# Kernel optimization log

Hardware: AMD Instinct MI355X
Metric: run time of the kernel (lower is better)

## Reference

```python
import jax, jax.numpy as jnp
import numpy as np

CLIP_TANH = 10.0
M_CHECKS, N_VARS = 256, 512   # parity-check matrix shape
ROW_W = 8                     # ones per check row -> E = 256*8 = 2048 edges
BATCH = 16384


def _build_masks():
    """Tanner-graph connectivity masks, as in init_w_skipconn2even / initialize_w_v2c."""
    rng = np.random.default_rng(0)
    pcm = np.zeros((M_CHECKS, N_VARS), np.float32)
    for r in range(M_CHECKS):
        pcm[r, rng.choice(N_VARS, ROW_W, replace=False)] = 1.0
    checks, variables = np.nonzero(pcm)  # edge list, row-major order, length E
    E = checks.size
    # edge e' feeds edge e iff same variable node, different check node
    same_var = variables[:, None] == variables[None, :]
    diff_chk = checks[:, None] != checks[None, :]
    w_odd2even_mask = (same_var & diff_chk).astype(np.float32)               # [E, E]
    # variable v feeds every edge incident to it
    w_skip_mask = (np.arange(N_VARS)[:, None] == variables[None, :]).astype(np.float32)  # [N, E]
    return jnp.asarray(w_odd2even_mask), jnp.asarray(w_skip_mask), E


def setup_inputs() -> dict:
    key = jax.random.key(0)
    w_o2e_mask, w_skip_mask, E = _build_masks()
    k = jax.random.split(key, 5)
    return {
        "x": jax.random.normal(k[0], (BATCH, E), jnp.float32),          # edge messages
        "llr": jax.random.normal(k[1], (BATCH, N_VARS), jnp.float32),   # channel LLRs
        "u": jax.random.uniform(k[2], (E,), jnp.float32),               # dropout uniforms
        "odd_weights": 0.05 * jax.random.normal(k[3], (E, E), jnp.float32),
        "llr_weights": 1.0 + 0.05 * jax.random.normal(k[4], (N_VARS, E), jnp.float32),
        "dropout_logits": 10.0 * jnp.ones((E,), jnp.float32),           # 10000*LOGITS_INIT analogue (sigmoid ~ 1)
        "w_odd2even_mask": w_o2e_mask,
        "w_skipconn2even_mask": w_skip_mask,
    }


def reference(x, llr, u, odd_weights, llr_weights, dropout_logits,
              w_odd2even_mask, w_skipconn2even_mask):
    # TEST-phase forward, mask_only=False
    total_mask = w_odd2even_mask * odd_weights                        # [E, E], very sparse support
    z = (u < jax.nn.sigmoid(dropout_logits)).astype(x.dtype)          # Bernoulli gate per source edge
    mask_after_dropout = total_mask * z[:, None]                      # row-wise gating
    msg = x @ mask_after_dropout                                      # [B, E]
    skip = llr @ (w_skipconn2even_mask * llr_weights)                 # [B, E]
    odd_clamp = jnp.clip(msg + skip, -CLIP_TANH, CLIP_TANH)
    return jnp.tanh(0.5 * odd_clamp)
```

## Files before the change

### kernel.cpp

```cpp
#include <hip/hip_runtime.h>
#include <hip/hip_bf16.h>

constexpr int E     = 2048;
constexpr int NVARS = 512;
constexpr int DMAX  = 20;
constexpr int TB    = 8;
constexpr int NT    = 512;

__device__ __forceinline__ unsigned bf16hi(float f) {
    const unsigned uu = __float_as_uint(f);
    return (uu + 0x7FFFu + ((uu >> 16) & 1u)) & 0xFFFF0000u;
}
__device__ __forceinline__ unsigned cvtpk(float lo, float hi) {
    unsigned r;
    asm("v_cvt_pk_bf16_f32 %0, %1, %2" : "=v"(r) : "v"(lo), "v"(hi));
    return r;
}
__device__ __forceinline__ float bl(unsigned q) { return __uint_as_float(q << 16); }
__device__ __forceinline__ float bh(unsigned q) { return __uint_as_float(q & 0xFFFF0000u); }

__global__ __launch_bounds__(256)
void k_vsrc(const float* __restrict__ skip_mask,
            const float* __restrict__ llr_w,
            unsigned short* __restrict__ vsrc,
            float* __restrict__ skw)
{
    const int col = blockIdx.x * 256 + threadIdx.x;
    const int v0  = blockIdx.y * (NVARS / 32);
    for (int v = v0; v < v0 + NVARS / 32; ++v) {
        const float m = skip_mask[(size_t)v * E + col];
        if (m != 0.0f) {
            vsrc[col] = (unsigned short)v;
            skw [col] = m * llr_w[(size_t)v * E + col];
        }
    }
}

__global__ __launch_bounds__(64)
void k_pervar(const unsigned short* __restrict__ vsrc,
              const float* __restrict__ skw,
              const float* __restrict__ odd_w,
              const float* __restrict__ u,
              const float* __restrict__ logits,
              uint4*  __restrict__ wtc,
              float4* __restrict__ hdr,
              int*    __restrict__ nitems)
{
    __shared__ unsigned short vs[E];
    __shared__ int deg[NVARS];
    __shared__ unsigned short mem[DMAX];
    __shared__ float zf[DMAX];
    __shared__ float sks[DMAX];

    const int v   = blockIdx.x;
    const int tid = threadIdx.x;

    for (int i = tid; i < E / 8; i += 64)
        ((uint4*)vs)[i] = ((const uint4*)vsrc)[i];
    for (int i = tid; i < NVARS; i += 64) deg[i] = 0;
    __syncthreads();
    for (int i = tid; i < E; i += 64) atomicAdd(&deg[vs[i]], 1);
    __syncthreads();

    const int dv = deg[v];

    int itot = 0, ib = 0, wb = 0;
    for (int i = tid; i < NVARS; i += 64) {
        const int d2 = deg[i];
        if (!d2) continue;
        const int dc = (d2 < DMAX) ? d2 : DMAX;
        const int ic = (dc + 3) >> 2;
        itot += ic;
        if (dv > 0 && (d2 < dv || (d2 == dv && i < v))) { ib += ic; wb += dc * ic; }
    }
    #pragma unroll
    for (int o = 32; o; o >>= 1) {
        itot += __shfl_xor(itot, o);
        ib   += __shfl_xor(ib,   o);
        wb   += __shfl_xor(wb,   o);
    }
    if (v == 0 && tid == 0) nitems[0] = itot;
    if (!dv) return;
    const int de = (dv < DMAX) ? dv : DMAX;
    const int ic = (de + 3) >> 2;

    int cnt = 0;
    for (int c = 0; c < E / 64; ++c) {
        const int e = c * 64 + tid;
        const bool m = ((int)vs[e] == v);
        const unsigned long long bal = __ballot(m);
        if (m) {
            const int pos = cnt + __popcll(bal & ((1ull << tid) - 1ull));
            if (pos < DMAX) mem[pos] = (unsigned short)e;
        }
        cnt += __popcll(bal);
    }
    __syncthreads();

    if (tid < de) {
        const int m = mem[tid];
        const float sig = 1.0f / (1.0f + __expf(-logits[m]));
        zf [tid] = (u[m] < sig) ? 1.0f : 0.0f;
        sks[tid] = skw[m];
    }
    __syncthreads();

    if (tid < ic) {
        const int o0 = tid * 4;
        float s0 = 0, s1 = 0, s2 = 0, s3 = 0;
        unsigned c0 = 0xFFFFu, c1 = 0xFFFFu, c2 = 0xFFFFu, c3 = 0xFFFFu;
        if (o0 + 0 < de) { s0 = sks[o0 + 0]; c0 = mem[o0 + 0]; }
        if (o0 + 1 < de) { s1 = sks[o0 + 1]; c1 = mem[o0 + 1]; }
        if (o0 + 2 < de) { s2 = sks[o0 + 2]; c2 = mem[o0 + 2]; }
        if (o0 + 3 < de) { s3 = sks[o0 + 3]; c3 = mem[o0 + 3]; }
        hdr[2 * (ib + tid)]     = make_float4(s0, s1, s2, s3);
        hdr[2 * (ib + tid) + 1] = make_float4(
            __uint_as_float(c0 | (c1 << 16)),
            __uint_as_float(c2 | (c3 << 16)),
            __uint_as_float((unsigned)(wb + tid * de)),
            __uint_as_float((unsigned)v | ((unsigned)de << 16)));
    }

    for (int idx = tid; idx < de * ic; idx += 64) {
        const int k = idx / de;
        const int j = idx - k * de;
        const int src = mem[j];
        unsigned g[4];
        #pragma unroll
        for (int q = 0; q < 4; ++q) {
            const int o = 4 * k + q;
            float ww = 0.0f;
            if (o < de && o != j)
                ww = odd_w[(size_t)src * E + mem[o]] * zf[j];
            g[q] = bf16hi(ww) | (unsigned)src;
        }
        wtc[wb + idx] = make_uint4(g[0], g[1], g[2], g[3]);
    }
}

__device__ __forceinline__ float th(float s) {
    float c = fminf(fmaxf(s, -10.0f), 10.0f);
    float t = __expf(c);
    return (t - 1.0f) * __frcp_rn(t + 1.0f);
}

__global__ __launch_bounds__(NT, 6)
void fused_main(const float* __restrict__ x,
                const float* __restrict__ llr,
                const uint4*  __restrict__ wtc,
                const float4* __restrict__ hdr,
                const int*    __restrict__ nitems,
                float* __restrict__ out)
{
    __shared__ uint4 xs[E];
    __shared__ uint4 ls[NVARS];

    const int b0 = blockIdx.x * TB;
    const int t  = threadIdx.x;

    {
        const float4* xr = (const float4*)(x + (size_t)b0 * E);
        const float4 r0 = xr[0 * (E / 4) + t];
        const float4 r1 = xr[1 * (E / 4) + t];
        const float4 r2 = xr[2 * (E / 4) + t];
        const float4 r3 = xr[3 * (E / 4) + t];
        const float4 r4 = xr[4 * (E / 4) + t];
        const float4 r5 = xr[5 * (E / 4) + t];
        const float4 r6 = xr[6 * (E / 4) + t];
        const float4 r7 = xr[7 * (E / 4) + t];
        xs[4 * t + 0] = make_uint4(cvtpk(r0.x, r1.x), cvtpk(r2.x, r3.x),
                                   cvtpk(r4.x, r5.x), cvtpk(r6.x, r7.x));
        xs[4 * t + 1] = make_uint4(cvtpk(r0.y, r1.y), cvtpk(r2.y, r3.y),
                                   cvtpk(r4.y, r5.y), cvtpk(r6.y, r7.y));
        xs[4 * t + 2] = make_uint4(cvtpk(r0.z, r1.z), cvtpk(r2.z, r3.z),
                                   cvtpk(r4.z, r5.z), cvtpk(r6.z, r7.z));
        xs[4 * t + 3] = make_uint4(cvtpk(r0.w, r1.w), cvtpk(r2.w, r3.w),
                                   cvtpk(r4.w, r5.w), cvtpk(r6.w, r7.w));
    }
    {
        const float* lr = llr + (size_t)b0 * NVARS;
        ls[t] = make_uint4(cvtpk(lr[t],             lr[NVARS + t]),
                           cvtpk(lr[2 * NVARS + t], lr[3 * NVARS + t]),
                           cvtpk(lr[4 * NVARS + t], lr[5 * NVARS + t]),
                           cvtpk(lr[6 * NVARS + t], lr[7 * NVARS + t]));
    }
    __syncthreads();

    const int nit = nitems[0];

    unsigned sst[2][4][4];
    unsigned scc[2][2];

    #pragma unroll
    for (int r = 0; r < 2; ++r) {
        scc[r][0] = 0xFFFFFFFFu;
        scc[r][1] = 0xFFFFFFFFu;
        const int it = r * NT + t;
        if (it < nit) {
            const float4 ha = hdr[2 * it];
            const uint4  hb = ((const uint4*)hdr)[2 * it + 1];
            const unsigned woff = hb.z;
            const int v = hb.w & 0xFFFF;
            const int d = hb.w >> 16;

            const uint4 lvq = ls[v];
            const float lf0 = bl(lvq.x), lf1 = bh(lvq.x);
            const float lf2 = bl(lvq.y), lf3 = bh(lvq.y);
            const float lf4 = bl(lvq.z), lf5 = bh(lvq.z);
            const float lf6 = bl(lvq.w), lf7 = bh(lvq.w);

            float a[4][8];
            #pragma unroll
            for (int ii = 0; ii < 4; ++ii) {
                const float sk = (ii == 0) ? ha.x : (ii == 1) ? ha.y
                               : (ii == 2) ? ha.z : ha.w;
                a[ii][0] = sk * lf0; a[ii][1] = sk * lf1;
                a[ii][2] = sk * lf2; a[ii][3] = sk * lf3;
                a[ii][4] = sk * lf4; a[ii][5] = sk * lf5;
                a[ii][6] = sk * lf6; a[ii][7] = sk * lf7;
            }

            const uint4* wp = wtc + woff;
            for (int j = 0; j < d; ++j) {
                const uint4 g = wp[j];
                const int   s = (int)(g.x & 0x7FFu);
                const uint4 xv = xs[s];
                const float w0 = bh(g.x), w1 = bh(g.y);
                const float w2 = bh(g.z), w3 = bh(g.w);
                const float xf0 = bl(xv.x), xf1 = bh(xv.x);
                const float xf2 = bl(xv.y), xf3 = bh(xv.y);
                const float xf4 = bl(xv.z), xf5 = bh(xv.z);
                const float xf6 = bl(xv.w), xf7 = bh(xv.w);
                a[0][0] += w0 * xf0; a[0][1] += w0 * xf1;
                a[0][2] += w0 * xf2; a[0][3] += w0 * xf3;
                a[0][4] += w0 * xf4; a[0][5] += w0 * xf5;
                a[0][6] += w0 * xf6; a[0][7] += w0 * xf7;
                a[1][0] += w1 * xf0; a[1][1] += w1 * xf1;
                a[1][2] += w1 * xf2; a[1][3] += w1 * xf3;
                a[1][4] += w1 * xf4; a[1][5] += w1 * xf5;
                a[1][6] += w1 * xf6; a[1][7] += w1 * xf7;
                a[2][0] += w2 * xf0; a[2][1] += w2 * xf1;
                a[2][2] += w2 * xf2; a[2][3] += w2 * xf3;
                a[2][4] += w2 * xf4; a[2][5] += w2 * xf5;
                a[2][6] += w2 * xf6; a[2][7] += w2 * xf7;
                a[3][0] += w3 * xf0; a[3][1] += w3 * xf1;
                a[3][2] += w3 * xf2; a[3][3] += w3 * xf3;
                a[3][4] += w3 * xf4; a[3][5] += w3 * xf5;
                a[3][6] += w3 * xf6; a[3][7] += w3 * xf7;
            }

            scc[r][0] = hb.x;
            scc[r][1] = hb.y;
            #pragma unroll
            for (int ii = 0; ii < 4; ++ii) {
                sst[r][ii][0] = cvtpk(th(a[ii][0]), th(a[ii][1]));
                sst[r][ii][1] = cvtpk(th(a[ii][2]), th(a[ii][3]));
                sst[r][ii][2] = cvtpk(th(a[ii][4]), th(a[ii][5]));
                sst[r][ii][3] = cvtpk(th(a[ii][6]), th(a[ii][7]));
            }
        }
    }

    __syncthreads();
    unsigned* osp = (unsigned*)xs;
    #pragma unroll
    for (int r = 0; r < 2; ++r) {
        #pragma unroll
        for (int ii = 0; ii < 4; ++ii) {
            const unsigned c = (scc[r][ii >> 1] >> ((ii & 1) * 16)) & 0xFFFFu;
            if (c != 0xFFFFu) {
                osp[0 * E + c] = sst[r][ii][0];
                osp[1 * E + c] = sst[r][ii][1];
                osp[2 * E + c] = sst[r][ii][2];
                osp[3 * E + c] = sst[r][ii][3];
            }
        }
    }
    __syncthreads();

    #pragma unroll
    for (int k = 0; k < E / NT; ++k) {
        const int e = k * NT + t;
        #pragma unroll
        for (int p = 0; p < 4; ++p) {
            const unsigned q = osp[p * E + e];
            out[(size_t)(b0 + 2 * p) * E + e]     = bl(q);
            out[(size_t)(b0 + 2 * p + 1) * E + e] = bh(q);
        }
    }
}

extern "C" void kernel_launch(void* const* d_in, const int* in_sizes, int n_in,
                              void* d_out, int out_size, void* d_ws, size_t ws_size,
                              hipStream_t stream) {
    const float* x        = (const float*)d_in[0];
    const float* llr      = (const float*)d_in[1];
    const float* u        = (const float*)d_in[2];
    const float* odd_w    = (const float*)d_in[3];
    const float* llr_w    = (const float*)d_in[4];
    const float* logits   = (const float*)d_in[5];
    const float* skip_msk = (const float*)d_in[7];
    float* out = (float*)d_out;

    const int B = in_sizes[0] / E;

    char* wsb = (char*)d_ws;
    size_t off = 0;
    uint4*          wtc  = (uint4*)(wsb + off);          off += (size_t)6144 * 16;
    float4*         hdr  = (float4*)(wsb + off);         off += (size_t)1024 * 32;
    float*          skw  = (float*)(wsb + off);          off += (size_t)E * 4;
    unsigned short* vsrc = (unsigned short*)(wsb + off); off += (size_t)E * 2;
    int*            nit  = (int*)(wsb + off);            off += 16;

    k_vsrc  <<<dim3(E / 256, 32), dim3(256), 0, stream>>>(skip_msk, llr_w, vsrc, skw);
    k_pervar<<<dim3(NVARS),       dim3(64),  0, stream>>>(vsrc, skw, odd_w, u, logits,
                                                          wtc, hdr, nit);

    fused_main<<<dim3(B / TB), dim3(NT), 0, stream>>>(x, llr, wtc, hdr, nit, out);
}
```

Baseline: 96.52 us.

## Prefetch first work item, software-pipeline gather loop, vectorize output stores

Several changes to the fused kernel. The first item's header and its first two weight entries are now loaded before the shared-memory staging barrier, so their global latency overlaps the x/llr conversion. The inner gather loop is software-pipelined so the next weight entry and its shared-memory x row are loaded before the current FMAs run. The output writeback now uses row-per-wavefront float4 stores instead of scalar strided stores, and the tanh reciprocal uses the raw hardware rcp. Together these aim to hide load latency and cut store instructions, at the cost of more live registers and a loop that reads one weight entry past the current item's degree.

```diff
diff --git a/kernel.cpp b/kernel.cpp
--- a/kernel.cpp
+++ b/kernel.cpp
@@ -141,8 +141,34 @@
 __device__ __forceinline__ float th(float s) {
     float c = fminf(fmaxf(s, -10.0f), 10.0f);
     float t = __expf(c);
-    return (t - 1.0f) * __frcp_rn(t + 1.0f);
-}
+    return (t - 1.0f) * __builtin_amdgcn_rcpf(t + 1.0f);
+}
+
+#define FMA8(gq, xvq)                                                         \
+    {                                                                         \
+        const float w0 = bh((gq).x), w1 = bh((gq).y);                         \
+        const float w2 = bh((gq).z), w3 = bh((gq).w);                         \
+        const float xf0 = bl((xvq).x), xf1 = bh((xvq).x);                     \
+        const float xf2 = bl((xvq).y), xf3 = bh((xvq).y);                     \
+        const float xf4 = bl((xvq).z), xf5 = bh((xvq).z);                     \
+        const float xf6 = bl((xvq).w), xf7 = bh((xvq).w);                     \
+        a[0][0] += w0 * xf0; a[0][1] += w0 * xf1;                             \
+        a[0][2] += w0 * xf2; a[0][3] += w0 * xf3;                             \
+        a[0][4] += w0 * xf4; a[0][5] += w0 * xf5;                             \
+        a[0][6] += w0 * xf6; a[0][7] += w0 * xf7;                             \
+        a[1][0] += w1 * xf0; a[1][1] += w1 * xf1;                             \
+        a[1][2] += w1 * xf2; a[1][3] += w1 * xf3;                             \
+        a[1][4] += w1 * xf4; a[1][5] += w1 * xf5;                             \
+        a[1][6] += w1 * xf6; a[1][7] += w1 * xf7;                             \
+        a[2][0] += w2 * xf0; a[2][1] += w2 * xf1;                             \
+        a[2][2] += w2 * xf2; a[2][3] += w2 * xf3;                             \
+        a[2][4] += w2 * xf4; a[2][5] += w2 * xf5;                             \
+        a[2][6] += w2 * xf6; a[2][7] += w2 * xf7;                             \
+        a[3][0] += w3 * xf0; a[3][1] += w3 * xf1;                             \
+        a[3][2] += w3 * xf2; a[3][3] += w3 * xf3;                             \
+        a[3][4] += w3 * xf4; a[3][5] += w3 * xf5;                             \
+        a[3][6] += w3 * xf6; a[3][7] += w3 * xf7;                             \
+    }
 
 __global__ __launch_bounds__(NT, 6)
 void fused_main(const float* __restrict__ x,
@@ -157,107 +183,131 @@
 
     const int b0 = blockIdx.x * TB;
     const int t  = threadIdx.x;
-
-    {
-        const float4* xr = (const float4*)(x + (size_t)b0 * E);
-        const float4 r0 = xr[0 * (E / 4) + t];
-        const float4 r1 = xr[1 * (E / 4) + t];
-        const float4 r2 = xr[2 * (E / 4) + t];
-        const float4 r3 = xr[3 * (E / 4) + t];
-        const float4 r4 = xr[4 * (E / 4) + t];
-        const float4 r5 = xr[5 * (E / 4) + t];
-        const float4 r6 = xr[6 * (E / 4) + t];
-        const float4 r7 = xr[7 * (E / 4) + t];
-        xs[4 * t + 0] = make_uint4(cvtpk(r0.x, r1.x), cvtpk(r2.x, r3.x),
-                                   cvtpk(r4.x, r5.x), cvtpk(r6.x, r7.x));
-        xs[4 * t + 1] = make_uint4(cvtpk(r0.y, r1.y), cvtpk(r2.y, r3.y),
-                                   cvtpk(r4.y, r5.y), cvtpk(r6.y, r7.y));
-        xs[4 * t + 2] = make_uint4(cvtpk(r0.z, r1.z), cvtpk(r2.z, r3.z),
-                                   cvtpk(r4.z, r5.z), cvtpk(r6.z, r7.z));
-        xs[4 * t + 3] = make_uint4(cvtpk(r0.w, r1.w), cvtpk(r2.w, r3.w),
-                                   cvtpk(r4.w, r5.w), cvtpk(r6.w, r7.w));
-    }
-    {
-        const float* lr = llr + (size_t)b0 * NVARS;
-        ls[t] = make_uint4(cvtpk(lr[t],             lr[NVARS + t]),
-                           cvtpk(lr[2 * NVARS + t], lr[3 * NVARS + t]),
-                           cvtpk(lr[4 * NVARS + t], lr[5 * NVARS + t]),
-                           cvtpk(lr[6 * NVARS + t], lr[7 * NVARS + t]));
-    }
-    __syncthreads();
-
     const int nit = nitems[0];
+
+    const float4* xr = (const float4*)(x + (size_t)b0 * E);
+    const float4 r0 = xr[0 * (E / 4) + t];
+    const float4 r1 = xr[1 * (E / 4) + t];
+    const float4 r2 = xr[2 * (E / 4) + t];
+    const float4 r3 = xr[3 * (E / 4) + t];
+    const float4 r4 = xr[4 * (E / 4) + t];
+    const float4 r5 = xr[5 * (E / 4) + t];
+    const float4 r6 = xr[6 * (E / 4) + t];
+    const float4 r7 = xr[7 * (E / 4) + t];
+    const float* lr = llr + (size_t)b0 * NVARS;
+    const float l0 = lr[t],             l1 = lr[NVARS + t];
+    const float l2 = lr[2 * NVARS + t], l3 = lr[3 * NVARS + t];
+    const float l4 = lr[4 * NVARS + t], l5 = lr[5 * NVARS + t];
+    const float l6 = lr[6 * NVARS + t], l7 = lr[7 * NVARS + t];
+
+    const float4 ha0 = hdr[2 * t];
+    const uint4  hb0 = ((const uint4*)hdr)[2 * t + 1];
+    const uint4* wp0 = wtc + hb0.z;
+    const uint4  g00 = wp0[0];
+    const uint4  g01 = wp0[1];
+
+    xs[4 * t + 0] = make_uint4(cvtpk(r0.x, r1.x), cvtpk(r2.x, r3.x),
+                               cvtpk(r4.x, r5.x), cvtpk(r6.x, r7.x));
+    xs[4 * t + 1] = make_uint4(cvtpk(r0.y, r1.y), cvtpk(r2.y, r3.y),
+                               cvtpk(r4.y, r5.y), cvtpk(r6.y, r7.y));
+    xs[4 * t + 2] = make_uint4(cvtpk(r0.z, r1.z), cvtpk(r2.z, r3.z),
+                               cvtpk(r4.z, r5.z), cvtpk(r6.z, r7.z));
+    xs[4 * t + 3] = make_uint4(cvtpk(r0.w, r1.w), cvtpk(r2.w, r3.w),
+                               cvtpk(r4.w, r5.w), cvtpk(r6.w, r7.w));
+    ls[t] = make_uint4(cvtpk(l0, l1), cvtpk(l2, l3),
+                       cvtpk(l4, l5), cvtpk(l6, l7));
+    __syncthreads();
 
     unsigned sst[2][4][4];
     unsigned scc[2][2];
 
-    #pragma unroll
-    for (int r = 0; r < 2; ++r) {
-        scc[r][0] = 0xFFFFFFFFu;
-        scc[r][1] = 0xFFFFFFFFu;
-        const int it = r * NT + t;
-        if (it < nit) {
-            const float4 ha = hdr[2 * it];
-            const uint4  hb = ((const uint4*)hdr)[2 * it + 1];
-            const unsigned woff = hb.z;
-            const int v = hb.w & 0xFFFF;
-            const int d = hb.w >> 16;
-
-            const uint4 lvq = ls[v];
-            const float lf0 = bl(lvq.x), lf1 = bh(lvq.x);
-            const float lf2 = bl(lvq.y), lf3 = bh(lvq.y);
-            const float lf4 = bl(lvq.z), lf5 = bh(lvq.z);
-            const float lf6 = bl(lvq.w), lf7 = bh(lvq.w);
-
-            float a[4][8];
-            #pragma unroll
-            for (int ii = 0; ii < 4; ++ii) {
-                const float sk = (ii == 0) ? ha.x : (ii == 1) ? ha.y
-                               : (ii == 2) ? ha.z : ha.w;
-                a[ii][0] = sk * lf0; a[ii][1] = sk * lf1;
-                a[ii][2] = sk * lf2; a[ii][3] = sk * lf3;
-                a[ii][4] = sk * lf4; a[ii][5] = sk * lf5;
-                a[ii][6] = sk * lf6; a[ii][7] = sk * lf7;
-            }
-
-            const uint4* wp = wtc + woff;
-            for (int j = 0; j < d; ++j) {
-                const uint4 g = wp[j];
-                const int   s = (int)(g.x & 0x7FFu);
-                const uint4 xv = xs[s];
-                const float w0 = bh(g.x), w1 = bh(g.y);
-                const float w2 = bh(g.z), w3 = bh(g.w);
-                const float xf0 = bl(xv.x), xf1 = bh(xv.x);
-                const float xf2 = bl(xv.y), xf3 = bh(xv.y);
-                const float xf4 = bl(xv.z), xf5 = bh(xv.z);
-                const float xf6 = bl(xv.w), xf7 = bh(xv.w);
-                a[0][0] += w0 * xf0; a[0][1] += w0 * xf1;
-                a[0][2] += w0 * xf2; a[0][3] += w0 * xf3;
-                a[0][4] += w0 * xf4; a[0][5] += w0 * xf5;
-                a[0][6] += w0 * xf6; a[0][7] += w0 * xf7;
-                a[1][0] += w1 * xf0; a[1][1] += w1 * xf1;
-                a[1][2] += w1 * xf2; a[1][3] += w1 * xf3;
-                a[1][4] += w1 * xf4; a[1][5] += w1 * xf5;
-                a[1][6] += w1 * xf6; a[1][7] += w1 * xf7;
-                a[2][0] += w2 * xf0; a[2][1] += w2 * xf1;
-                a[2][2] += w2 * xf2; a[2][3] += w2 * xf3;
-                a[2][4] += w2 * xf4; a[2][5] += w2 * xf5;
-                a[2][6] += w2 * xf6; a[2][7] += w2 * xf7;
-                a[3][0] += w3 * xf0; a[3][1] += w3 * xf1;
-                a[3][2] += w3 * xf2; a[3][3] += w3 * xf3;
-                a[3][4] += w3 * xf4; a[3][5] += w3 * xf5;
-                a[3][6] += w3 * xf6; a[3][7] += w3 * xf7;
-            }
-
-            scc[r][0] = hb.x;
-            scc[r][1] = hb.y;
-            #pragma unroll
-            for (int ii = 0; ii < 4; ++ii) {
-                sst[r][ii][0] = cvtpk(th(a[ii][0]), th(a[ii][1]));
-                sst[r][ii][1] = cvtpk(th(a[ii][2]), th(a[ii][3]));
-                sst[r][ii][2] = cvtpk(th(a[ii][4]), th(a[ii][5]));
-                sst[r][ii][3] = cvtpk(th(a[ii][6]), th(a[ii][7]));
-            }
+    {
+        const int v = hb0.w & 0xFFFF;
+        const int d = hb0.w >> 16;
+
+        const uint4 lvq = ls[v];
+        const float lf0 = bl(lvq.x), lf1 = bh(lvq.x);
+        const float lf2 = bl(lvq.y), lf3 = bh(lvq.y);
+        const float lf4 = bl(lvq.z), lf5 = bh(lvq.z);
+        const float lf6 = bl(lvq.w), lf7 = bh(lvq.w);
+
+        float a[4][8];
+        #pragma unroll
+        for (int ii = 0; ii < 4; ++ii) {
+            const float sk = (ii == 0) ? ha0.x : (ii == 1) ? ha0.y
+                           : (ii == 2) ? ha0.z : ha0.w;
+            a[ii][0] = sk * lf0; a[ii][1] = sk * lf1;
+            a[ii][2] = sk * lf2; a[ii][3] = sk * lf3;
+            a[ii][4] = sk * lf4; a[ii][5] = sk * lf5;
+            a[ii][6] = sk * lf6; a[ii][7] = sk * lf7;
+        }
+
+        uint4 gc = g00, gn = g01;
+        uint4 xc = xs[gc.x & 0x7FFu];
+        for (int j = 0; j < d - 1; ++j) {
+            const uint4 gf = wp0[j + 2];
+            const uint4 xn = xs[gn.x & 0x7FFu];
+            FMA8(gc, xc);
+            gc = gn; xc = xn; gn = gf;
+        }
+        FMA8(gc, xc);
+
+        scc[0][0] = hb0.x;
+        scc[0][1] = hb0.y;
+        #pragma unroll
+        for (int ii = 0; ii < 4; ++ii) {
+            sst[0][ii][0] = cvtpk(th(a[ii][0]), th(a[ii][1]));
+            sst[0][ii][1] = cvtpk(th(a[ii][2]), th(a[ii][3]));
+            sst[0][ii][2] = cvtpk(th(a[ii][4]), th(a[ii][5]));
+            sst[0][ii][3] = cvtpk(th(a[ii][6]), th(a[ii][7]));
+        }
+    }
+
+    scc[1][0] = 0xFFFFFFFFu;
+    scc[1][1] = 0xFFFFFFFFu;
+    if (NT + t < nit) {
+        const int it = NT + t;
+        const float4 ha1 = hdr[2 * it];
+        const uint4  hb1 = ((const uint4*)hdr)[2 * it + 1];
+        const uint4* wp1 = wtc + hb1.z;
+        const int v = hb1.w & 0xFFFF;
+        const int d = hb1.w >> 16;
+
+        const uint4 lvq = ls[v];
+        const float lf0 = bl(lvq.x), lf1 = bh(lvq.x);
+        const float lf2 = bl(lvq.y), lf3 = bh(lvq.y);
+        const float lf4 = bl(lvq.z), lf5 = bh(lvq.z);
+        const float lf6 = bl(lvq.w), lf7 = bh(lvq.w);
+
+        float a[4][8];
+        #pragma unroll
+        for (int ii = 0; ii < 4; ++ii) {
+            const float sk = (ii == 0) ? ha1.x : (ii == 1) ? ha1.y
+                           : (ii == 2) ? ha1.z : ha1.w;
+            a[ii][0] = sk * lf0; a[ii][1] = sk * lf1;
+            a[ii][2] = sk * lf2; a[ii][3] = sk * lf3;
+            a[ii][4] = sk * lf4; a[ii][5] = sk * lf5;
+            a[ii][6] = sk * lf6; a[ii][7] = sk * lf7;
+        }
+
+        uint4 gc = wp1[0], gn = wp1[1];
+        uint4 xc = xs[gc.x & 0x7FFu];
+        for (int j = 0; j < d - 1; ++j) {
+            const uint4 gf = wp1[j + 2];
+            const uint4 xn = xs[gn.x & 0x7FFu];
+            FMA8(gc, xc);
+            gc = gn; xc = xn; gn = gf;
+        }
+        FMA8(gc, xc);
+
+        scc[1][0] = hb1.x;
+        scc[1][1] = hb1.y;
+        #pragma unroll
+        for (int ii = 0; ii < 4; ++ii) {
+            sst[1][ii][0] = cvtpk(th(a[ii][0]), th(a[ii][1]));
+            sst[1][ii][1] = cvtpk(th(a[ii][2]), th(a[ii][3]));
+            sst[1][ii][2] = cvtpk(th(a[ii][4]), th(a[ii][5]));
+            sst[1][ii][3] = cvtpk(th(a[ii][6]), th(a[ii][7]));
         }
     }
 
@@ -278,14 +328,21 @@
     }
     __syncthreads();
 
-    #pragma unroll
-    for (int k = 0; k < E / NT; ++k) {
-        const int e = k * NT + t;
-        #pragma unroll
-        for (int p = 0; p < 4; ++p) {
-            const unsigned q = osp[p * E + e];
-            out[(size_t)(b0 + 2 * p) * E + e]     = bl(q);
-            out[(size_t)(b0 + 2 * p + 1) * E + e] = bh(q);
+    {
+        const int row = t >> 6, l = t & 63;
+        const int p = row >> 1, hf = row & 1;
+        float* orow = out + (size_t)(b0 + row) * E;
+        const uint4* plane = (const uint4*)(osp + p * E);
+        #pragma unroll
+        for (int i = 0; i < 8; ++i) {
+            const int q4 = i * 64 + l;
+            const uint4 w4 = plane[q4];
+            float4 o;
+            if (hf == 0)
+                o = make_float4(bl(w4.x), bl(w4.y), bl(w4.z), bl(w4.w));
+            else
+                o = make_float4(bh(w4.x), bh(w4.y), bh(w4.z), bh(w4.w));
+            ((float4*)orow)[q4] = o;
         }
     }
 }
```

Result: no change. 96.74 us (+0.2%).
